# Optimization experiments

Hardware: AMD Instinct MI355X
Metric: run time of the kernel (lower is better)

Reference implementation:

```python
import jax, jax.numpy as jnp
import numpy as np

B, C_IN, C_OUT, H, W = 16, 192, 192, 128, 128
K_EXPERTS, LATENT_DIM = 8, 64


def setup_inputs() -> dict:
    key = jax.random.key(0)
    ks = jax.random.split(key, 6)
    s = lambda fan: np.float32(1.0 / np.sqrt(fan))
    return {
        "x": jax.random.normal(ks[0], (B, C_IN, H, W), jnp.float32),
        "latent": jax.random.normal(ks[1], (B, LATENT_DIM), jnp.float32),
        # DyConv2d: K expert 3x3 kernels + biases, attention FC from latent
        "expert_w": jax.random.normal(ks[2], (K_EXPERTS, C_OUT, C_IN, 3, 3), jnp.float32) * s(C_IN * 9),
        "expert_b": jnp.zeros((K_EXPERTS, C_OUT), jnp.float32),
        "attn_w": jax.random.normal(ks[3], (K_EXPERTS, LATENT_DIM), jnp.float32) * s(LATENT_DIM),
        "attn_b": jnp.zeros((K_EXPERTS,), jnp.float32),
        # static conv2 (3x3) weights
        "conv2_w": jax.random.normal(ks[4], (C_OUT, C_OUT, 3, 3), jnp.float32) * s(C_OUT * 9),
        "conv2_b": jnp.zeros((C_OUT,), jnp.float32),
    }


def _conv3x3(x, w, b):
    # x: [N,C,H,W], w: [O,I,3,3] -> [N,O,H,W]
    y = jax.lax.conv_general_dilated(
        x, w, window_strides=(1, 1), padding=((1, 1), (1, 1)),
        dimension_numbers=("NCHW", "OIHW", "NCHW"))
    return y + b[None, :, None, None]


def reference(x, latent, expert_w, expert_b, attn_w, attn_b, conv2_w, conv2_b):
    identity = x  # stride=1, in_ch==out_ch -> adaptor is None
    # ---- DyConv2d: latent -> expert attention -> per-sample kernel ----
    attn = jax.nn.softmax(latent @ attn_w.T + attn_b, axis=-1)        # [B,K]
    w_dyn = jnp.einsum("bk,koihw->boihw", attn, expert_w)            # [B,O,I,3,3]
    b_dyn = attn @ expert_b                                          # [B,O]
    # per-sample conv, vectorized over batch
    out = jax.vmap(lambda xi, wi, bi: _conv3x3(xi[None], wi, bi)[0])(x, w_dyn, b_dyn)
    out = jax.nn.silu(out)
    # ---- static conv3x3 ----
    out = _conv3x3(out, conv2_w, conv2_b)
    out = jax.nn.silu(out)
    return out + identity
```

## Files before the change

### kernel.cpp

```cpp
#include <hip/hip_runtime.h>
#include <stdint.h>
#include <stddef.h>

typedef __bf16 bf16;
typedef bf16 bf16x8 __attribute__((ext_vector_type(8)));
typedef bf16 bf16x4 __attribute__((ext_vector_type(4)));
typedef float f32x4 __attribute__((ext_vector_type(4)));
typedef float f32x16 __attribute__((ext_vector_type(16)));

#define B_   16
#define CI   192
#define CO   192
#define H_   128
#define W_   128
#define KE   8
#define LD   64
#define KTOT 1728
#define HP   130
#define HPHP (HP*HP)
#define NPX  (H_*W_)
#define NT   54

__device__ __forceinline__ void gll16(const void* g, void* l) {
  __builtin_amdgcn_global_load_lds(
      (const __attribute__((address_space(1))) unsigned int*)g,
      (__attribute__((address_space(3))) unsigned int*)l, 16, 0, 0);
}

__device__ __forceinline__ float silu_f(float x) {
  return x / (1.f + __expf(-x));
}

__device__ __forceinline__ void attn_inline(const float* __restrict__ latent,
                                            const float* __restrict__ attn_w,
                                            const float* __restrict__ attn_b,
                                            float (*al)[KE], int tid) {
  if (tid < 128) {
    int b = tid >> 3, k = tid & 7;
    float s = attn_b[k];
    #pragma unroll 8
    for (int d = 0; d < LD; ++d) s += latent[b*LD + d] * attn_w[k*LD + d];
    float m = s;
    for (int off = 4; off; off >>= 1) m = fmaxf(m, __shfl_xor(m, off, 8));
    float e = __expf(s - m);
    float sum = e;
    for (int off = 4; off; off >>= 1) sum += __shfl_xor(sum, off, 8);
    al[b][k] = e / sum;
  }
  __syncthreads();
}

__global__ void k_bdyn(const float* __restrict__ latent, const float* __restrict__ attn_w,
                       const float* __restrict__ attn_b, const float* __restrict__ expert_b,
                       float* __restrict__ bdyn) {
  __shared__ float al[B_][KE];
  attn_inline(latent, attn_w, attn_b, al, threadIdx.x);
  int j = blockIdx.x * 256 + threadIdx.x;
  if (j >= B_ * CO) return;
  int b = j / CO, o = j - b * CO;
  float s = 0.f;
  #pragma unroll
  for (int e = 0; e < KE; ++e) s += al[b][e] * expert_b[e*CO + o];
  bdyn[j] = s;
}

__global__ void k_wdyn(const float* __restrict__ expert_w, const float* __restrict__ latent,
                       const float* __restrict__ attn_w, const float* __restrict__ attn_b,
                       bf16* __restrict__ w_re) {
  int o = blockIdx.x;
  int chunk = o >> 4, row = o & 15, c = (row >> 1) & 3;
  __shared__ float ew[KE][KTOT];
  __shared__ float al[B_][KE];
  attn_inline(latent, attn_w, attn_b, al, threadIdx.x);
  for (int e = 0; e < KE; ++e)
    for (int j = threadIdx.x; j < KTOT; j += 256)
      ew[e][j] = expert_w[((size_t)e*CO + o)*KTOT + j];
  __syncthreads();
  for (int idx = threadIdx.x; idx < B_*KTOT; idx += 256) {
    int b = idx / KTOT, k = idx - b*KTOT;
    int kt = k >> 5, ks = (k >> 3) & 3, j = k & 7;
    int r = kt / 18, t2 = kt - r*18;
    int ibb = t2 / 3, s = t2 - ibb*3;
    int i = ibb*32 + ks*8 + j;
    float acc = 0.f;
    #pragma unroll
    for (int e = 0; e < KE; ++e) acc += al[b][e] * ew[e][i*9 + r*3 + s];
    int slot = row*4 + (ks ^ c);
    w_re[((((size_t)b*NT + kt)*12 + chunk)*64 + slot)*8 + j] = (bf16)acc;
  }
}

__global__ void k_w2re(const float* __restrict__ conv2_w, bf16* __restrict__ w2_re) {
  int o = blockIdx.x;
  int chunk = o >> 4, row = o & 15, c = (row >> 1) & 3;
  __shared__ float cw[KTOT];
  for (int j = threadIdx.x; j < KTOT; j += 256) cw[j] = conv2_w[(size_t)o*KTOT + j];
  __syncthreads();
  for (int k = threadIdx.x; k < KTOT; k += 256) {
    int kt = k >> 5, ks = (k >> 3) & 3, j = k & 7;
    int r = kt / 18, t2 = kt - r*18;
    int ibb = t2 / 3, s = t2 - ibb*3;
    int i = ibb*32 + ks*8 + j;
    int slot = row*4 + (ks ^ c);
    w2_re[(((size_t)kt*12 + chunk)*64 + slot)*8 + j] = (bf16)cw[i*9 + r*3 + s];
  }
}

__global__ void k_xpack(const float* __restrict__ x, bf16* __restrict__ xpack,
                        bf16* __restrict__ midpack) {
  int h2 = blockIdx.x, ib = blockIdx.y, b = blockIdx.z;
  size_t rowbase = (((size_t)b*24 + ib)*HP + h2)*HP;
  int t = threadIdx.x;
  uint4 z = make_uint4(0,0,0,0);
  if (h2 == 0 || h2 == HP-1) {
    for (int w = t; w < HP; w += 128) {
      *(uint4*)(xpack   + (rowbase + w)*8) = z;
      *(uint4*)(midpack + (rowbase + w)*8) = z;
    }
    return;
  }
  __shared__ float tt[8][128];
  int h = h2 - 1;
  #pragma unroll
  for (int ii = 0; ii < 8; ++ii)
    tt[ii][t] = x[(((size_t)b*CI + ib*8 + ii)*H_ + h)*W_ + t];
  __syncthreads();
  bf16x8 v;
  #pragma unroll
  for (int ii = 0; ii < 8; ++ii) v[ii] = (bf16)tt[ii][t];
  *(bf16x8*)(xpack + (rowbase + t + 1)*8) = v;
  if (t == 0) {
    *(uint4*)(xpack + rowbase*8) = z;
    *(uint4*)(xpack + (rowbase + HP-1)*8) = z;
    *(uint4*)(midpack + rowbase*8) = z;
    *(uint4*)(midpack + (rowbase + HP-1)*8) = z;
  }
}

template<int MODE>
__global__ __launch_bounds__(256, 2)
void k_conv(const bf16* __restrict__ wre, const bf16* __restrict__ inpack,
            const float* __restrict__ bias_g, const bf16* __restrict__ respack,
            bf16* __restrict__ outpack, float* __restrict__ outp) {
  const int tid  = threadIdx.x;
  const int lane = tid & 63;
  const int wv   = tid >> 6;
  const int wm   = wv >> 1;
  const int wn   = wv & 1;
  const int l15  = lane & 15;
  const int l31  = lane & 31;
  const int lhi  = lane >> 5;

  const int bid  = blockIdx.x;
  const int n    = (bid & 7) * 128 + (bid >> 3);
  const int b    = n >> 6;
  const int tile = n & 63;
  const int p0   = tile * 256;
  const int h0   = tile * 2;

  __shared__ __align__(16) bf16 Alds[3][12*512];
  __shared__ __align__(16) bf16 Blds[2][4*2560];
  __shared__ float bias_lds[CO];

  if (tid < CO) bias_lds[tid] = (MODE == 0) ? bias_g[b*CO + tid] : bias_g[tid];

  const size_t wbase = (MODE == 0) ? ((size_t)b*CO*KTOT) : 0;

  const bf16* aS = wre + wbase + (size_t)wv*512 + lane*8;
  const bf16* bbase = inpack + (((size_t)b*24 + wv)*HPHP + (size_t)h0*HP)*8 + lane*8;
  int ibm = 0; ptrdiff_t boffEl = 0;

  auto stageA = [&](bf16* dbuf) {
    bf16* d = dbuf + wv*512;
    gll16(aS,        d);
    gll16(aS + 2048, d + 2048);
    gll16(aS + 4096, d + 4096);
    aS += 6144;
  };
  auto stageB = [&](bf16* dbuf) {
    const bf16* src = bbase + boffEl;
    bf16* d = dbuf + wv*2560;
    gll16(src,        d);
    gll16(src +  512, d +  512);
    gll16(src + 1024, d + 1024);
    gll16(src + 1536, d + 1536);
    gll16(src + 1568, d + 1568);
    if (++ibm == 6) { ibm = 0; boffEl += (ptrdiff_t)(HP - 20*HPHP)*8; }
    else boffEl += (ptrdiff_t)4*HPHP*8;
  };

  f32x16 acc[3][4];
  #pragma unroll
  for (int mt = 0; mt < 3; ++mt)
    #pragma unroll
    for (int nt = 0; nt < 4; ++nt)
      #pragma unroll
      for (int jj = 0; jj < 16; ++jj) acc[mt][nt][jj] = 0.f;

  const int arow   = l15;
  const int aswz   = (arow >> 1) & 3;
  const int achnk  = (lane >> 4) & 1;
  const int aoff0  = arow*32 + ((lhi       ^ aswz) * 8);
  const int aoff1  = arow*32 + (((2 + lhi) ^ aswz) * 8);
  const int bcol   = (wn*130 + l31) * 8;
  const int bkg    = lhi * 2560;

  stageB(Blds[0]);
  stageA(Alds[0]);
  stageA(Alds[1]);

  bf16* Bcur = (bf16*)Blds[0];
  bf16* Bnxt = (bf16*)Blds[1];

  for (int m = 0; m < 18; ++m) {
    #pragma unroll
    for (int s = 0; s < 3; ++s) {
      if (s == 2) {
        if (m == 17) asm volatile("s_waitcnt vmcnt(0)" ::: "memory");
        else         asm volatile("s_waitcnt vmcnt(8)" ::: "memory");
      } else {
        asm volatile("s_waitcnt vmcnt(3)" ::: "memory");
      }
      __builtin_amdgcn_s_barrier();

      const bf16* A  = Alds[s];
      const bf16* bp = Bcur + bkg + bcol + s*8;

      bf16x8 a0 = *(const bf16x8*)(A + (wm*6 + 0 + achnk)*512 + aoff0);
      bf16x8 a1 = *(const bf16x8*)(A + (wm*6 + 2 + achnk)*512 + aoff0);
      bf16x8 a2 = *(const bf16x8*)(A + (wm*6 + 4 + achnk)*512 + aoff0);
      bf16x8 b0 = *(const bf16x8*)(bp);
      bf16x8 b1 = *(const bf16x8*)(bp + 256);
      bf16x8 b2 = *(const bf16x8*)(bp + 512);
      bf16x8 b3 = *(const bf16x8*)(bp + 768);

      if (3*m + s + 2 < NT) stageA(Alds[(s+2)%3]);

      __builtin_amdgcn_s_barrier();
      __builtin_amdgcn_s_setprio(1);
      acc[0][0] = __builtin_amdgcn_mfma_f32_32x32x16_bf16(a0, b0, acc[0][0], 0, 0, 0);
      acc[0][1] = __builtin_amdgcn_mfma_f32_32x32x16_bf16(a0, b1, acc[0][1], 0, 0, 0);
      acc[0][2] = __builtin_amdgcn_mfma_f32_32x32x16_bf16(a0, b2, acc[0][2], 0, 0, 0);
      acc[0][3] = __builtin_amdgcn_mfma_f32_32x32x16_bf16(a0, b3, acc[0][3], 0, 0, 0);
      acc[1][0] = __builtin_amdgcn_mfma_f32_32x32x16_bf16(a1, b0, acc[1][0], 0, 0, 0);
      acc[1][1] = __builtin_amdgcn_mfma_f32_32x32x16_bf16(a1, b1, acc[1][1], 0, 0, 0);
      acc[1][2] = __builtin_amdgcn_mfma_f32_32x32x16_bf16(a1, b2, acc[1][2], 0, 0, 0);
      acc[1][3] = __builtin_amdgcn_mfma_f32_32x32x16_bf16(a1, b3, acc[1][3], 0, 0, 0);
      acc[2][0] = __builtin_amdgcn_mfma_f32_32x32x16_bf16(a2, b0, acc[2][0], 0, 0, 0);
      acc[2][1] = __builtin_amdgcn_mfma_f32_32x32x16_bf16(a2, b1, acc[2][1], 0, 0, 0);
      acc[2][2] = __builtin_amdgcn_mfma_f32_32x32x16_bf16(a2, b2, acc[2][2], 0, 0, 0);
      acc[2][3] = __builtin_amdgcn_mfma_f32_32x32x16_bf16(a2, b3, acc[2][3], 0, 0, 0);
      __builtin_amdgcn_s_setprio(0);

      bf16x8 a3 = *(const bf16x8*)(A + (wm*6 + 0 + achnk)*512 + aoff1);
      bf16x8 a4 = *(const bf16x8*)(A + (wm*6 + 2 + achnk)*512 + aoff1);
      bf16x8 a5 = *(const bf16x8*)(A + (wm*6 + 4 + achnk)*512 + aoff1);
      bf16x8 b4 = *(const bf16x8*)(bp + 2*2560);
      bf16x8 b5 = *(const bf16x8*)(bp + 2*2560 + 256);
      bf16x8 b6 = *(const bf16x8*)(bp + 2*2560 + 512);
      bf16x8 b7 = *(const bf16x8*)(bp + 2*2560 + 768);

      if (s == 1 && m < 17) stageB(Bnxt);

      __builtin_amdgcn_s_barrier();
      __builtin_amdgcn_s_setprio(1);
      acc[0][0] = __builtin_amdgcn_mfma_f32_32x32x16_bf16(a3, b4, acc[0][0], 0, 0, 0);
      acc[0][1] = __builtin_amdgcn_mfma_f32_32x32x16_bf16(a3, b5, acc[0][1], 0, 0, 0);
      acc[0][2] = __builtin_amdgcn_mfma_f32_32x32x16_bf16(a3, b6, acc[0][2], 0, 0, 0);
      acc[0][3] = __builtin_amdgcn_mfma_f32_32x32x16_bf16(a3, b7, acc[0][3], 0, 0, 0);
      acc[1][0] = __builtin_amdgcn_mfma_f32_32x32x16_bf16(a4, b4, acc[1][0], 0, 0, 0);
      acc[1][1] = __builtin_amdgcn_mfma_f32_32x32x16_bf16(a4, b5, acc[1][1], 0, 0, 0);
      acc[1][2] = __builtin_amdgcn_mfma_f32_32x32x16_bf16(a4, b6, acc[1][2], 0, 0, 0);
      acc[1][3] = __builtin_amdgcn_mfma_f32_32x32x16_bf16(a4, b7, acc[1][3], 0, 0, 0);
      acc[2][0] = __builtin_amdgcn_mfma_f32_32x32x16_bf16(a5, b4, acc[2][0], 0, 0, 0);
      acc[2][1] = __builtin_amdgcn_mfma_f32_32x32x16_bf16(a5, b5, acc[2][1], 0, 0, 0);
      acc[2][2] = __builtin_amdgcn_mfma_f32_32x32x16_bf16(a5, b6, acc[2][2], 0, 0, 0);
      acc[2][3] = __builtin_amdgcn_mfma_f32_32x32x16_bf16(a5, b7, acc[2][3], 0, 0, 0);
      __builtin_amdgcn_s_setprio(0);
    }
    { bf16* t = Bcur; Bcur = Bnxt; Bnxt = t; }
  }

  #pragma unroll
  for (int mt = 0; mt < 3; ++mt) {
    #pragma unroll
    for (int nt = 0; nt < 4; ++nt) {
      int w = nt*32 + l31;
      int p = p0 + wn*128 + w;
      #pragma unroll
      for (int rq = 0; rq < 4; ++rq) {
        int ob = wm*96 + mt*32 + rq*8 + 4*lhi;
        size_t basep = (((size_t)b*24 + (ob >> 3))*HP + (h0 + wn + 1))*HP + (w + 1);
        if (MODE == 0) {
          bf16x4 pk;
          #pragma unroll
          for (int jj = 0; jj < 4; ++jj) {
            float xv = acc[mt][nt][rq*4 + jj] + bias_lds[ob + jj];
            pk[jj] = (bf16)silu_f(xv);
          }
          *(bf16x4*)(outpack + basep*8 + (ob & 7)) = pk;
        } else {
          bf16x4 rr = *(const bf16x4*)(respack + basep*8 + (ob & 7));
          #pragma unroll
          for (int jj = 0; jj < 4; ++jj) {
            float xv = silu_f(acc[mt][nt][rq*4 + jj] + bias_lds[ob + jj]);
            size_t idx = ((size_t)b*CO + ob + jj)*NPX + p;
            outp[idx] = xv + (float)rr[jj];
          }
        }
      }
    }
  }
}

extern "C" void kernel_launch(void* const* d_in, const int* in_sizes, int n_in,
                              void* d_out, int out_size, void* d_ws, size_t ws_size,
                              hipStream_t stream) {
  const float* x        = (const float*)d_in[0];
  const float* latent   = (const float*)d_in[1];
  const float* expert_w = (const float*)d_in[2];
  const float* expert_b = (const float*)d_in[3];
  const float* attn_w   = (const float*)d_in[4];
  const float* attn_b   = (const float*)d_in[5];
  const float* conv2_w  = (const float*)d_in[6];
  const float* conv2_b  = (const float*)d_in[7];
  float* outp = (float*)d_out;

  char* base = (char*)d_ws;
  size_t off = 0;
  float* bdyn = (float*)(base + off); off += 16384;
  bf16* w_re  = (bf16*)(base + off);  off += (size_t)B_*CO*KTOT*2;
  bf16* w2_re = (bf16*)(base + off);  off += (size_t)CO*KTOT*2;
  bf16* xpack = (bf16*)(base + off);  off += (size_t)B_*24*HPHP*8*2;
  bf16* midpack = (bf16*)(base + off); off += (size_t)B_*24*HPHP*8*2;
  (void)ws_size; (void)in_sizes; (void)n_in; (void)out_size;

  k_xpack<<<dim3(130, 24, 16), dim3(128), 0, stream>>>(x, xpack, midpack);
  k_wdyn<<<dim3(CO), dim3(256), 0, stream>>>(expert_w, latent, attn_w, attn_b, w_re);
  k_bdyn<<<dim3(12), dim3(256), 0, stream>>>(latent, attn_w, attn_b, expert_b, bdyn);
  k_w2re<<<dim3(CO), dim3(256), 0, stream>>>(conv2_w, w2_re);
  k_conv<0><<<dim3(1024), dim3(256), 0, stream>>>(w_re, xpack, bdyn, xpack, midpack, outp);
  k_conv<1><<<dim3(1024), dim3(256), 0, stream>>>(w2_re, midpack, conv2_b, xpack, midpack, outp);
}
```

Before: 459.9 us.

## Halve conv output tile to one image row per block, doubling grid

```diff
diff --git a/kernel.cpp b/kernel.cpp
--- a/kernel.cpp
+++ b/kernel.cpp
@@ -152,14 +152,12 @@
   const int lhi  = lane >> 5;
 
   const int bid  = blockIdx.x;
-  const int n    = (bid & 7) * 128 + (bid >> 3);
-  const int b    = n >> 6;
-  const int tile = n & 63;
-  const int p0   = tile * 256;
-  const int h0   = tile * 2;
+  const int n    = (bid & 7) * 256 + (bid >> 3);
+  const int b    = n >> 7;
+  const int row  = n & 127;
 
   __shared__ __align__(16) bf16 Alds[3][12*512];
-  __shared__ __align__(16) bf16 Blds[2][4*2560];
+  __shared__ __align__(16) bf16 Blds[2][4*1040];
   __shared__ float bias_lds[CO];
 
   if (tid < CO) bias_lds[tid] = (MODE == 0) ? bias_g[b*CO + tid] : bias_g[tid];
@@ -167,7 +165,7 @@
   const size_t wbase = (MODE == 0) ? ((size_t)b*CO*KTOT) : 0;
 
   const bf16* aS = wre + wbase + (size_t)wv*512 + lane*8;
-  const bf16* bbase = inpack + (((size_t)b*24 + wv)*HPHP + (size_t)h0*HP)*8 + lane*8;
+  const bf16* bbase = inpack + (((size_t)b*24 + wv)*HPHP + (size_t)row*HP)*8 + lane*8;
   int ibm = 0; ptrdiff_t boffEl = 0;
 
   auto stageA = [&](bf16* dbuf) {
@@ -179,21 +177,19 @@
   };
   auto stageB = [&](bf16* dbuf) {
     const bf16* src = bbase + boffEl;
-    bf16* d = dbuf + wv*2560;
-    gll16(src,        d);
-    gll16(src +  512, d +  512);
-    gll16(src + 1024, d + 1024);
-    gll16(src + 1536, d + 1536);
-    gll16(src + 1568, d + 1568);
+    bf16* d = dbuf + wv*1040;
+    gll16(src,       d);
+    gll16(src + 512, d + 512);
+    gll16(src + 528, d + 528);
     if (++ibm == 6) { ibm = 0; boffEl += (ptrdiff_t)(HP - 20*HPHP)*8; }
     else boffEl += (ptrdiff_t)4*HPHP*8;
   };
 
-  f32x16 acc[3][4];
+  f32x16 acc[3][2];
   #pragma unroll
   for (int mt = 0; mt < 3; ++mt)
     #pragma unroll
-    for (int nt = 0; nt < 4; ++nt)
+    for (int nt = 0; nt < 2; ++nt)
       #pragma unroll
       for (int jj = 0; jj < 16; ++jj) acc[mt][nt][jj] = 0.f;
 
@@ -202,8 +198,8 @@
   const int achnk  = (lane >> 4) & 1;
   const int aoff0  = arow*32 + ((lhi       ^ aswz) * 8);
   const int aoff1  = arow*32 + (((2 + lhi) ^ aswz) * 8);
-  const int bcol   = (wn*130 + l31) * 8;
-  const int bkg    = lhi * 2560;
+  const int bcol   = (wn*64 + l31) * 8;
+  const int bkg    = lhi * 1040;
 
   stageB(Blds[0]);
   stageA(Alds[0]);
@@ -217,7 +213,7 @@
     for (int s = 0; s < 3; ++s) {
       if (s == 2) {
         if (m == 17) asm volatile("s_waitcnt vmcnt(0)" ::: "memory");
-        else         asm volatile("s_waitcnt vmcnt(8)" ::: "memory");
+        else         asm volatile("s_waitcnt vmcnt(6)" ::: "memory");
       } else {
         asm volatile("s_waitcnt vmcnt(3)" ::: "memory");
       }
@@ -231,8 +227,6 @@
       bf16x8 a2 = *(const bf16x8*)(A + (wm*6 + 4 + achnk)*512 + aoff0);
       bf16x8 b0 = *(const bf16x8*)(bp);
       bf16x8 b1 = *(const bf16x8*)(bp + 256);
-      bf16x8 b2 = *(const bf16x8*)(bp + 512);
-      bf16x8 b3 = *(const bf16x8*)(bp + 768);
 
       if (3*m + s + 2 < NT) stageA(Alds[(s+2)%3]);
 
@@ -240,42 +234,28 @@
       __builtin_amdgcn_s_setprio(1);
       acc[0][0] = __builtin_amdgcn_mfma_f32_32x32x16_bf16(a0, b0, acc[0][0], 0, 0, 0);
       acc[0][1] = __builtin_amdgcn_mfma_f32_32x32x16_bf16(a0, b1, acc[0][1], 0, 0, 0);
-      acc[0][2] = __builtin_amdgcn_mfma_f32_32x32x16_bf16(a0, b2, acc[0][2], 0, 0, 0);
-      acc[0][3] = __builtin_amdgcn_mfma_f32_32x32x16_bf16(a0, b3, acc[0][3], 0, 0, 0);
       acc[1][0] = __builtin_amdgcn_mfma_f32_32x32x16_bf16(a1, b0, acc[1][0], 0, 0, 0);
       acc[1][1] = __builtin_amdgcn_mfma_f32_32x32x16_bf16(a1, b1, acc[1][1], 0, 0, 0);
-      acc[1][2] = __builtin_amdgcn_mfma_f32_32x32x16_bf16(a1, b2, acc[1][2], 0, 0, 0);
-      acc[1][3] = __builtin_amdgcn_mfma_f32_32x32x16_bf16(a1, b3, acc[1][3], 0, 0, 0);
       acc[2][0] = __builtin_amdgcn_mfma_f32_32x32x16_bf16(a2, b0, acc[2][0], 0, 0, 0);
       acc[2][1] = __builtin_amdgcn_mfma_f32_32x32x16_bf16(a2, b1, acc[2][1], 0, 0, 0);
-      acc[2][2] = __builtin_amdgcn_mfma_f32_32x32x16_bf16(a2, b2, acc[2][2], 0, 0, 0);
-      acc[2][3] = __builtin_amdgcn_mfma_f32_32x32x16_bf16(a2, b3, acc[2][3], 0, 0, 0);
       __builtin_amdgcn_s_setprio(0);
 
       bf16x8 a3 = *(const bf16x8*)(A + (wm*6 + 0 + achnk)*512 + aoff1);
       bf16x8 a4 = *(const bf16x8*)(A + (wm*6 + 2 + achnk)*512 + aoff1);
       bf16x8 a5 = *(const bf16x8*)(A + (wm*6 + 4 + achnk)*512 + aoff1);
-      bf16x8 b4 = *(const bf16x8*)(bp + 2*2560);
-      bf16x8 b5 = *(const bf16x8*)(bp + 2*2560 + 256);
-      bf16x8 b6 = *(const bf16x8*)(bp + 2*2560 + 512);
-      bf16x8 b7 = *(const bf16x8*)(bp + 2*2560 + 768);
+      bf16x8 b2 = *(const bf16x8*)(bp + 2*1040);
+      bf16x8 b3 = *(const bf16x8*)(bp + 2*1040 + 256);
 
       if (s == 1 && m < 17) stageB(Bnxt);
 
       __builtin_amdgcn_s_barrier();
       __builtin_amdgcn_s_setprio(1);
-      acc[0][0] = __builtin_amdgcn_mfma_f32_32x32x16_bf16(a3, b4, acc[0][0], 0, 0, 0);
-      acc[0][1] = __builtin_amdgcn_mfma_f32_32x32x16_bf16(a3, b5, acc[0][1], 0, 0, 0);
-      acc[0][2] = __builtin_amdgcn_mfma_f32_32x32x16_bf16(a3, b6, acc[0][2], 0, 0, 0);
-      acc[0][3] = __builtin_amdgcn_mfma_f32_32x32x16_bf16(a3, b7, acc[0][3], 0, 0, 0);
-      acc[1][0] = __builtin_amdgcn_mfma_f32_32x32x16_bf16(a4, b4, acc[1][0], 0, 0, 0);
-      acc[1][1] = __builtin_amdgcn_mfma_f32_32x32x16_bf16(a4, b5, acc[1][1], 0, 0, 0);
-      acc[1][2] = __builtin_amdgcn_mfma_f32_32x32x16_bf16(a4, b6, acc[1][2], 0, 0, 0);
-      acc[1][3] = __builtin_amdgcn_mfma_f32_32x32x16_bf16(a4, b7, acc[1][3], 0, 0, 0);
-      acc[2][0] = __builtin_amdgcn_mfma_f32_32x32x16_bf16(a5, b4, acc[2][0], 0, 0, 0);
-      acc[2][1] = __builtin_amdgcn_mfma_f32_32x32x16_bf16(a5, b5, acc[2][1], 0, 0, 0);
-      acc[2][2] = __builtin_amdgcn_mfma_f32_32x32x16_bf16(a5, b6, acc[2][2], 0, 0, 0);
-      acc[2][3] = __builtin_amdgcn_mfma_f32_32x32x16_bf16(a5, b7, acc[2][3], 0, 0, 0);
+      acc[0][0] = __builtin_amdgcn_mfma_f32_32x32x16_bf16(a3, b2, acc[0][0], 0, 0, 0);
+      acc[0][1] = __builtin_amdgcn_mfma_f32_32x32x16_bf16(a3, b3, acc[0][1], 0, 0, 0);
+      acc[1][0] = __builtin_amdgcn_mfma_f32_32x32x16_bf16(a4, b2, acc[1][0], 0, 0, 0);
+      acc[1][1] = __builtin_amdgcn_mfma_f32_32x32x16_bf16(a4, b3, acc[1][1], 0, 0, 0);
+      acc[2][0] = __builtin_amdgcn_mfma_f32_32x32x16_bf16(a5, b2, acc[2][0], 0, 0, 0);
+      acc[2][1] = __builtin_amdgcn_mfma_f32_32x32x16_bf16(a5, b3, acc[2][1], 0, 0, 0);
       __builtin_amdgcn_s_setprio(0);
     }
     { bf16* t = Bcur; Bcur = Bnxt; Bnxt = t; }
@@ -284,13 +264,13 @@
   #pragma unroll
   for (int mt = 0; mt < 3; ++mt) {
     #pragma unroll
-    for (int nt = 0; nt < 4; ++nt) {
-      int w = nt*32 + l31;
-      int p = p0 + wn*128 + w;
+    for (int nt = 0; nt < 2; ++nt) {
+      int w = wn*64 + nt*32 + l31;
+      int p = row*128 + w;
       #pragma unroll
       for (int rq = 0; rq < 4; ++rq) {
         int ob = wm*96 + mt*32 + rq*8 + 4*lhi;
-        size_t basep = (((size_t)b*24 + (ob >> 3))*HP + (h0 + wn + 1))*HP + (w + 1);
+        size_t basep = (((size_t)b*24 + (ob >> 3))*HP + (row + 1))*HP + (w + 1);
         if (MODE == 0) {
           bf16x4 pk;
           #pragma unroll
@@ -339,6 +319,6 @@
   k_wdyn<<<dim3(CO), dim3(256), 0, stream>>>(expert_w, latent, attn_w, attn_b, w_re);
   k_bdyn<<<dim3(12), dim3(256), 0, stream>>>(latent, attn_w, attn_b, expert_b, bdyn);
   k_w2re<<<dim3(CO), dim3(256), 0, stream>>>(conv2_w, w2_re);
-  k_conv<0><<<dim3(1024), dim3(256), 0, stream>>>(w_re, xpack, bdyn, xpack, midpack, outp);
-  k_conv<1><<<dim3(1024), dim3(256), 0, stream>>>(w2_re, midpack, conv2_b, xpack, midpack, outp);
-}
+  k_conv<0><<<dim3(2048), dim3(256), 0, stream>>>(w_re, xpack, bdyn, xpack, midpack, outp);
+  k_conv<1><<<dim3(2048), dim3(256), 0, stream>>>(w2_re, midpack, conv2_b, xpack, midpack, outp);
+}
```

New measurement: 511.8 us. 11.3% more time.
